# Performance work log

Hardware: AMD Instinct MI355X
Metric: run time of the kernel (lower is better)

The kernel has to match this reference:

```python
import jax, jax.numpy as jnp
import numpy as np

N, F_IN, C, H, E, B = 100000, 128, 64, 4, 1200000, 8
NEG_SLOPE = 0.2
EPS = 1e-5


def setup_inputs() -> dict:
    key = jax.random.key(0)
    ks = jax.random.split(key, 12)
    x = jax.random.normal(ks[0], (N, F_IN), dtype=jnp.float32)
    edge_index = jax.random.randint(ks[1], (2, E), 0, N, dtype=jnp.int64)
    batch = jnp.sort(jax.random.randint(ks[2], (N,), 0, B, dtype=jnp.int64))
    # GATConv params (lin has no bias in PyG)
    W = jax.random.normal(ks[3], (H * C, F_IN), dtype=jnp.float32) / np.sqrt(F_IN)
    att_src = jax.random.normal(ks[4], (H, C), dtype=jnp.float32) / np.sqrt(C)
    att_dst = jax.random.normal(ks[5], (H, C), dtype=jnp.float32) / np.sqrt(C)
    bias_gat = jax.random.normal(ks[6], (C,), dtype=jnp.float32) * 0.02
    # residual projection (in != out)
    res_W = jax.random.normal(ks[7], (C, F_IN), dtype=jnp.float32) / np.sqrt(F_IN)
    res_b = jax.random.normal(ks[8], (C,), dtype=jnp.float32) * 0.02
    # GraphNorm params
    gn_weight = jnp.ones((C,), dtype=jnp.float32) + 0.1 * jax.random.normal(ks[9], (C,), dtype=jnp.float32)
    gn_bias = 0.02 * jax.random.normal(ks[10], (C,), dtype=jnp.float32)
    gn_mean_scale = jnp.ones((C,), dtype=jnp.float32) + 0.1 * jax.random.normal(ks[11], (C,), dtype=jnp.float32)
    return {"x": x, "edge_index": edge_index, "batch": batch, "W": W,
            "att_src": att_src, "att_dst": att_dst, "bias_gat": bias_gat,
            "res_W": res_W, "res_b": res_b, "gn_weight": gn_weight,
            "gn_bias": gn_bias, "gn_mean_scale": gn_mean_scale}


def reference(x, edge_index, batch, W, att_src, att_dst, bias_gat,
              res_W, res_b, gn_weight, gn_bias, gn_mean_scale):
    n = x.shape[0]
    residual = x @ res_W.T + res_b                      # [N, C]
    xl = (x @ W.T).reshape(n, H, C)                     # [N, H, C]
    a_src = jnp.einsum('nhc,hc->nh', xl, att_src)       # [N, H]
    a_dst = jnp.einsum('nhc,hc->nh', xl, att_dst)
    # add self loops
    loop = jnp.arange(n, dtype=edge_index.dtype)
    src = jnp.concatenate([edge_index[0], loop])        # [E+N]
    dst = jnp.concatenate([edge_index[1], loop])
    alpha = jax.nn.leaky_relu(a_src[src] + a_dst[dst], NEG_SLOPE)  # [E+N, H]
    # segment softmax over incoming edges per destination node
    amax = jax.ops.segment_max(alpha, dst, num_segments=n)
    ex = jnp.exp(alpha - amax[dst])
    denom = jax.ops.segment_sum(ex, dst, num_segments=n)
    coef = ex / denom[dst]                              # [E+N, H]
    msg = coef[:, :, None] * xl[src]                    # [E+N, H, C]
    agg = jax.ops.segment_sum(msg, dst, num_segments=n) # [N, H, C]
    out = agg.mean(axis=1) + bias_gat                   # concat=False -> head mean
    h = out + residual
    # GraphNorm over per-graph segments
    cnt = jax.ops.segment_sum(jnp.ones((n,), h.dtype), batch, num_segments=B)[:, None]  # [B,1]
    mean = jax.ops.segment_sum(h, batch, num_segments=B) / cnt                          # [B,C]
    centered = h - mean[batch] * gn_mean_scale
    var = jax.ops.segment_sum(centered * centered, batch, num_segments=B) / cnt         # [B,C]
    normed = gn_weight * centered / jnp.sqrt(var[batch] + EPS) + gn_bias
    return jax.nn.gelu(normed)  # dropout is identity in eval
```

## Files before the change

kernel.cpp:

```cpp
#include <hip/hip_runtime.h>
#include <hip/hip_bf16.h>

typedef __bf16 bf16;
typedef __bf16 bf16x4 __attribute__((ext_vector_type(4)));
typedef __bf16 bf16x8 __attribute__((ext_vector_type(8)));
typedef float floatx4 __attribute__((ext_vector_type(4)));
typedef _Float16 f16;
typedef _Float16 f16x4 __attribute__((ext_vector_type(4)));
typedef _Float16 h2 __attribute__((ext_vector_type(2)));

#define FIN 128
#define HC 256
#define HEADS 4
#define CDIM 64
#define BGRAPH 8
#define NEG 0.2f
#define EPS_GN 1e-5f
#define CAP 48


__device__ __forceinline__ float lrelu(float v) { return v >= 0.f ? v : NEG * v; }
__device__ __forceinline__ float eexp(float v) { return __expf(fminf(v, 60.f)); }

__device__ __forceinline__ float dot2h(h2 a, h2 b, float c) {
#if __has_builtin(__builtin_amdgcn_fdot2)
    return __builtin_amdgcn_fdot2(a, b, c, false);
#else
    return c + (float)a[0] * (float)b[0] + (float)a[1] * (float)b[1];
#endif
}
__device__ __forceinline__ h2 bch2(unsigned u) { return __builtin_bit_cast(h2, u); }

__device__ __forceinline__ bool sniff_i64(const int* __restrict__ p) {
    bool w64 = true;
#pragma unroll
    for (int i = 1; i < 16; i += 2) w64 = w64 && (p[i] == 0);
    return w64;
}
__device__ __forceinline__ bool sniff_f32(const void* __restrict__ xv) {
    const unsigned* u = (const unsigned*)xv;
    bool bf = true;
#pragma unroll
    for (int i = 0; i < 8; ++i) {
        unsigned lo = u[i] & 0xFFFFu;
        unsigned ex = (lo >> 7) & 0xFFu;
        bf = bf && ((ex >= 96u && ex <= 129u) || lo == 0u);
    }
    return !bf;
}

__device__ __forceinline__ int gidx(const int* __restrict__ p, long long i,
                                    bool w64, int hi) {
    long long v = w64 ? ((const long long*)p)[i] : (long long)p[i];
    int x = (int)v;
    return x < 0 ? 0 : (x >= hi ? hi - 1 : x);
}

template <bool F32>
__device__ __forceinline__ float ldf(const void* __restrict__ p, int i) {
    if constexpr (F32) return ((const float*)p)[i];
    else               return (float)((const bf16*)p)[i];
}

template <bool F32>
__device__ __forceinline__ bf16x8 load8(const void* __restrict__ base, size_t off) {
    if constexpr (F32) {
        const float* p = (const float*)base + off;
        float4 a = *(const float4*)p, b = *(const float4*)(p + 4);
        bf16x8 r;
        r[0] = (bf16)a.x; r[1] = (bf16)a.y; r[2] = (bf16)a.z; r[3] = (bf16)a.w;
        r[4] = (bf16)b.x; r[5] = (bf16)b.y; r[6] = (bf16)b.z; r[7] = (bf16)b.w;
        return r;
    } else {
        return *(const bf16x8*)((const bf16*)base + off);
    }
}

template <bool F32>
__device__ __forceinline__ void k1_impl(
        const void* __restrict__ x, const bf16x8* __restrict__ Wlds,
        const void* __restrict__ resW, const void* __restrict__ resB,
        const void* __restrict__ biasG,
        const bf16* __restrict__ aSc, const bf16* __restrict__ aDc,
        f16* __restrict__ xl, float* __restrict__ out_acc,
        float* __restrict__ a_src, float* __restrict__ a_dst, int N) {
    const int wave = threadIdx.x >> 6;
    const int lane = threadIdx.x & 63;
    const int nl = lane & 15;
    const int q  = lane >> 4;
    const int base = blockIdx.x * 128 + wave * 32;

    bf16x8 xf[2][4];
    int nodes[2]; bool g[2];
#pragma unroll
    for (int nt = 0; nt < 2; ++nt) {
        int node = base + nt * 16 + nl;
        nodes[nt] = node; g[nt] = node < N;
        int cn = g[nt] ? node : N - 1;
#pragma unroll
        for (int kq = 0; kq < 4; ++kq)
            xf[nt][kq] = load8<F32>(x, (size_t)cn * FIN + kq * 32 + q * 8);
    }

    float s[2][4] = {{0,0,0,0},{0,0,0,0}};
    float d[2][4] = {{0,0,0,0},{0,0,0,0}};

#pragma unroll
    for (int tile = 0; tile < 16; ++tile) {
        bf16x8 wf[4];
#pragma unroll
        for (int kq = 0; kq < 4; ++kq)
            wf[kq] = Wlds[(tile * 4 + kq) * 64 + lane];
        const int e0 = tile * 16 + q * 4;
        bf16x4 sa = *(const bf16x4*)(aSc + e0);
        bf16x4 da = *(const bf16x4*)(aDc + e0);
#pragma unroll
        for (int nt = 0; nt < 2; ++nt) {
            floatx4 acc = {0,0,0,0};
#pragma unroll
            for (int kq = 0; kq < 4; ++kq)
                acc = __builtin_amdgcn_mfma_f32_16x16x32_bf16(wf[kq], xf[nt][kq], acc, 0, 0, 0);
            f16x4 p;
#pragma unroll
            for (int r = 0; r < 4; ++r) {
                p[r] = (f16)acc[r];
                s[nt][r] += acc[r] * (float)sa[r];
                d[nt][r] += acc[r] * (float)da[r];
            }
            if (g[nt]) *(f16x4*)(xl + (size_t)nodes[nt] * HC + e0) = p;
        }
    }

#pragma unroll
    for (int tile = 0; tile < 4; ++tile) {
        const int R = tile * 16 + nl;
        bf16x8 wf[4];
#pragma unroll
        for (int kq = 0; kq < 4; ++kq)
            wf[kq] = load8<F32>(resW, (size_t)R * FIN + kq * 32 + q * 8);
        const int c0 = tile * 16 + q * 4;
        const float b0 = ldf<F32>(resB, c0 + 0) + ldf<F32>(biasG, c0 + 0);
        const float b1 = ldf<F32>(resB, c0 + 1) + ldf<F32>(biasG, c0 + 1);
        const float b2 = ldf<F32>(resB, c0 + 2) + ldf<F32>(biasG, c0 + 2);
        const float b3 = ldf<F32>(resB, c0 + 3) + ldf<F32>(biasG, c0 + 3);
#pragma unroll
        for (int nt = 0; nt < 2; ++nt) {
            floatx4 acc = {0,0,0,0};
#pragma unroll
            for (int kq = 0; kq < 4; ++kq)
                acc = __builtin_amdgcn_mfma_f32_16x16x32_bf16(wf[kq], xf[nt][kq], acc, 0, 0, 0);
            float4 v = make_float4(acc[0] + b0, acc[1] + b1, acc[2] + b2, acc[3] + b3);
            if (g[nt]) *(float4*)(out_acc + (size_t)nodes[nt] * CDIM + c0) = v;
        }
    }

#pragma unroll
    for (int off = 16; off <= 32; off <<= 1) {
#pragma unroll
        for (int nt = 0; nt < 2; ++nt)
#pragma unroll
            for (int r = 0; r < 4; ++r) {
                s[nt][r] += __shfl_xor(s[nt][r], off, 64);
                d[nt][r] += __shfl_xor(d[nt][r], off, 64);
            }
    }
    if (q == 0) {
#pragma unroll
        for (int nt = 0; nt < 2; ++nt) {
            if (g[nt]) {
                *(float4*)(a_src + (size_t)nodes[nt] * 4) =
                    make_float4(s[nt][0], s[nt][1], s[nt][2], s[nt][3]);
                *(float4*)(a_dst + (size_t)nodes[nt] * 4) =
                    make_float4(d[nt][0], d[nt][1], d[nt][2], d[nt][3]);
            }
        }
    }
}

__global__ __launch_bounds__(256, 2) void k1_gemm(
        const void* __restrict__ x, const void* __restrict__ W,
        const void* __restrict__ resW, const void* __restrict__ resB,
        const void* __restrict__ biasG, const void* __restrict__ attS,
        const void* __restrict__ attD,
        f16* __restrict__ xl, float* __restrict__ out_acc,
        float* __restrict__ a_src, float* __restrict__ a_dst,
        int* __restrict__ cnt, int N) {
    __shared__ bf16x8 Wlds[4096];
    __shared__ bf16 aSc[HC], aDc[HC];
    const bool f32 = sniff_f32(x);
    const int t = threadIdx.x;
    {
        int gid = blockIdx.x * 256 + t;
        if (gid < N) cnt[gid] = 0;
    }
    {
        int src = (t & 3) * 64 + (t >> 2);
        aSc[t] = f32 ? (bf16)((const float*)attS)[src] : ((const bf16*)attS)[src];
        aDc[t] = f32 ? (bf16)((const float*)attD)[src] : ((const bf16*)attD)[src];
    }
    if (f32) {
#pragma unroll
        for (int j = 0; j < 16; ++j) {
            int i = t + j * 256;
            int tileq = i >> 6, lane = i & 63;
            int tile = tileq >> 2, kq = tileq & 3;
            int R = tile * 16 + (lane & 15);
            size_t off = (size_t)((R & 3) * 64 + (R >> 2)) * FIN + kq * 32 + (lane >> 4) * 8;
            Wlds[i] = load8<true>(W, off);
        }
    } else {
#pragma unroll
        for (int j = 0; j < 16; ++j) {
            int i = t + j * 256;
            int tileq = i >> 6, lane = i & 63;
            int tile = tileq >> 2, kq = tileq & 3;
            int R = tile * 16 + (lane & 15);
            size_t off = (size_t)((R & 3) * 64 + (R >> 2)) * FIN + kq * 32 + (lane >> 4) * 8;
            Wlds[i] = load8<false>(W, off);
        }
    }
    __syncthreads();
    if (f32) k1_impl<true >(x, Wlds, resW, resB, biasG, aSc, aDc, xl, out_acc, a_src, a_dst, N);
    else     k1_impl<false>(x, Wlds, resW, resB, biasG, aSc, aDc, xl, out_acc, a_src, a_dst, N);
}

__global__ __launch_bounds__(256) void kscat(
        const int* __restrict__ ei, int* __restrict__ cnt,
        int* __restrict__ adj, int E, int N) {
    int e = blockIdx.x * 256 + threadIdx.x;
    if (e >= E) return;
    bool w64 = sniff_i64(ei);
    int s = gidx(ei, e, w64, N);
    int d = gidx(ei, (long long)E + e, w64, N);
    int pos = atomicAdd(&cnt[d], 1);
    if (pos < CAP) adj[(size_t)d * CAP + pos] = s;
}

__global__ __launch_bounds__(256) void k3_fused(
        const int* __restrict__ cnt, const int* __restrict__ adj,
        const float* __restrict__ a_src, const float* __restrict__ a_dst,
        const f16* __restrict__ xl, float* __restrict__ out_acc, int N) {
    __shared__ unsigned sh_w[4][64][2];
    __shared__ int      sh_off[4][64];
    const int wid  = threadIdx.x >> 6;
    const int lane = threadIdx.x & 63;
    const int n = blockIdx.x * 4 + wid;
    if (n >= N) return;
    int cn = cnt[n]; if (cn > CAP) cn = CAP;
    const float4 ad  = *(const float4*)(a_dst + (size_t)n * 4);
    const float4 asn = *(const float4*)(a_src + (size_t)n * 4);
    const float e0 = eexp(lrelu(asn.x + ad.x));
    const float e1 = eexp(lrelu(asn.y + ad.y));
    const float e2 = eexp(lrelu(asn.z + ad.z));
    const float e3 = eexp(lrelu(asn.w + ad.w));

    float w0 = 0.f, w1 = 0.f, w2 = 0.f, w3 = 0.f;
    float d0 = 0.f, d1 = 0.f, d2 = 0.f, d3 = 0.f;
    int s = 0;
    if (lane < cn) {
        s = adj[(size_t)n * CAP + lane];
        float4 as = *(const float4*)(a_src + (size_t)s * 4);
        w0 = eexp(lrelu(as.x + ad.x));
        w1 = eexp(lrelu(as.y + ad.y));
        w2 = eexp(lrelu(as.z + ad.z));
        w3 = eexp(lrelu(as.w + ad.w));
        d0 = w0; d1 = w1; d2 = w2; d3 = w3;
    }
#pragma unroll
    for (int off = 1; off <= 32; off <<= 1) {
        d0 += __shfl_xor(d0, off, 64);
        d1 += __shfl_xor(d1, off, 64);
        d2 += __shfl_xor(d2, off, 64);
        d3 += __shfl_xor(d3, off, 64);
    }
    d0 += e0; d1 += e1; d2 += e2; d3 += e3;
    const float i0 = 0.25f * __builtin_amdgcn_rcpf(d0);
    const float i1 = 0.25f * __builtin_amdgcn_rcpf(d1);
    const float i2 = 0.25f * __builtin_amdgcn_rcpf(d2);
    const float i3 = 0.25f * __builtin_amdgcn_rcpf(d3);

    if (lane < cn) {
        h2 wa; wa[0] = (f16)(w0 * i0); wa[1] = (f16)(w1 * i1);
        h2 wb; wb[0] = (f16)(w2 * i2); wb[1] = (f16)(w3 * i3);
        sh_w[wid][lane][0] = __builtin_bit_cast(unsigned, wa);
        sh_w[wid][lane][1] = __builtin_bit_cast(unsigned, wb);
        sh_off[wid][lane] = s << 9;
    } else if (lane == cn) {
        h2 wa; wa[0] = (f16)(e0 * i0); wa[1] = (f16)(e1 * i1);
        h2 wb; wb[0] = (f16)(e2 * i2); wb[1] = (f16)(e3 * i3);
        sh_w[wid][cn][0] = __builtin_bit_cast(unsigned, wa);
        sh_w[wid][cn][1] = __builtin_bit_cast(unsigned, wb);
        sh_off[wid][cn] = n << 9;
    }

    const int m = cn + 1;
    const int half = lane >> 5, l32 = lane & 31;
    const char* xb = (const char*)xl + l32 * 16;
    float acc0 = 0.f, acc1 = 0.f;

#define K3DOT(raw, wr) do {                                              \
        h2 va = bch2((raw).x), vb = bch2((raw).y);                       \
        h2 vc = bch2((raw).z), vd = bch2((raw).w);                       \
        h2 wa = bch2((wr).x),  wb = bch2((wr).y);                        \
        acc0 = dot2h(va, wa, acc0); acc0 = dot2h(vb, wb, acc0);          \
        acc1 = dot2h(vc, wa, acc1); acc1 = dot2h(vd, wb, acc1);          \
    } while (0)

    int j = 0;
    for (; j + 4 <= m; j += 4) {
        int offA = sh_off[wid][j + half];
        int offB = sh_off[wid][j + 2 + half];
        uint4 ra = *(const uint4*)(xb + offA);
        uint4 rb = *(const uint4*)(xb + offB);
        uint2 wA = *(const uint2*)&sh_w[wid][j + half][0];
        uint2 wB = *(const uint2*)&sh_w[wid][j + 2 + half][0];
        K3DOT(ra, wA);
        K3DOT(rb, wB);
    }
    if (j + 2 <= m) {
        int offA = sh_off[wid][j + half];
        uint4 ra = *(const uint4*)(xb + offA);
        uint2 wA = *(const uint2*)&sh_w[wid][j + half][0];
        K3DOT(ra, wA);
        j += 2;
    }
    if (j < m && half == 0) {
        int offA = sh_off[wid][j];
        uint4 ra = *(const uint4*)(xb + offA);
        uint2 wA = *(const uint2*)&sh_w[wid][j][0];
        K3DOT(ra, wA);
    }
#undef K3DOT

    acc0 += __shfl_xor(acc0, 32, 64);
    acc1 += __shfl_xor(acc1, 32, 64);
    if (half == 0) {
        float2* p = (float2*)(out_acc + (size_t)n * CDIM + l32 * 2);
        float2 v = *p;
        v.x += acc0; v.y += acc1;
        *p = v;
    }
}

__global__ __launch_bounds__(256) void k4_stats(
        const float* __restrict__ out_acc, const int* __restrict__ batch,
        const int* __restrict__ ei,
        float* __restrict__ pS1, float* __restrict__ pS2, int N) {
    __shared__ float p1[4][BGRAPH][64], p2[4][BGRAPH][64];
    const int w = threadIdx.x >> 6;
    const int c = threadIdx.x & 63;
#pragma unroll
    for (int k = threadIdx.x; k < 4 * BGRAPH * 64; k += 256) {
        ((float*)p1)[k] = 0.f; ((float*)p2)[k] = 0.f;
    }
    __syncthreads();
    bool w64 = sniff_i64(ei);
    const int n0 = blockIdx.x * 256 + w * 64;
    float ls1 = 0.f, ls2 = 0.f;
    int curb = -1;
    for (int i = 0; i < 64; ++i) {
        int n = n0 + i;
        if (n >= N) break;
        float hv = out_acc[(size_t)n * CDIM + c];
        int b = gidx(batch, n, w64, BGRAPH);
        if (b != curb) {
            if (curb >= 0) { p1[w][curb][c] += ls1; p2[w][curb][c] += ls2; }
            curb = b; ls1 = 0.f; ls2 = 0.f;
        }
        ls1 += hv; ls2 += hv * hv;
    }
    if (curb >= 0) { p1[w][curb][c] += ls1; p2[w][curb][c] += ls2; }
    __syncthreads();
    for (int k = threadIdx.x; k < BGRAPH * 64; k += 256) {
        int b = k >> 6, cc = k & 63;
        pS1[(size_t)blockIdx.x * (BGRAPH * 64) + k] =
            p1[0][b][cc] + p1[1][b][cc] + p1[2][b][cc] + p1[3][b][cc];
        pS2[(size_t)blockIdx.x * (BGRAPH * 64) + k] =
            p2[0][b][cc] + p2[1][b][cc] + p2[2][b][cc] + p2[3][b][cc];
    }
}

__global__ __launch_bounds__(256) void kr_reduce(
        const float* __restrict__ pS1, const float* __restrict__ pS2,
        float* __restrict__ S1, float* __restrict__ S2,
        const int* __restrict__ batch, const int* __restrict__ ei,
        int* __restrict__ start, int nblk, int N) {
    __shared__ float r1[4][64], r2[4][64];
    const int b = blockIdx.x;
    const int seg = threadIdx.x >> 6;
    const int c = threadIdx.x & 63;
    float s1 = 0.f, s2 = 0.f;
    for (int blk = seg; blk < nblk; blk += 4) {
        s1 += pS1[(size_t)blk * (BGRAPH * 64) + b * 64 + c];
        s2 += pS2[(size_t)blk * (BGRAPH * 64) + b * 64 + c];
    }
    r1[seg][c] = s1; r2[seg][c] = s2;
    __syncthreads();
    if (seg == 0) {
        S1[b * 64 + c] = r1[0][c] + r1[1][c] + r1[2][c] + r1[3][c];
        S2[b * 64 + c] = r2[0][c] + r2[1][c] + r2[2][c] + r2[3][c];
    }
    if (b == 0 && threadIdx.x <= BGRAPH) {
        int t = threadIdx.x;
        bool w64 = sniff_i64(ei);
        int lo = 0, hi = N;
        while (lo < hi) {
            int mid = (lo + hi) >> 1;
            long long bv = w64 ? ((const long long*)batch)[mid] : (long long)batch[mid];
            if (bv < t) lo = mid + 1; else hi = mid;
        }
        start[t] = lo;
    }
}

template <bool F32>
__device__ __forceinline__ void k6_impl(
        const float* __restrict__ out_acc, const int* __restrict__ batch,
        bool w64,
        const float* __restrict__ S1, const float* __restrict__ S2,
        const int* __restrict__ start, const void* __restrict__ gw,
        const void* __restrict__ gb, const void* __restrict__ msc,
        void* __restrict__ out, int N) {
    int idx = blockIdx.x * 256 + threadIdx.x;
    if (idx >= N * CDIM) return;
    int n = idx >> 6, c = idx & 63;
    int b = gidx(batch, n, w64, BGRAPH);
    int cnt_i = start[b + 1] - start[b];
    float cnt = (float)(cnt_i < 1 ? 1 : cnt_i);
    float m = S1[b * CDIM + c] / cnt;
    float ms = ldf<F32>(msc, c);
    float var = S2[b * CDIM + c] / cnt + m * m * ms * (ms - 2.0f);
    float centered = out_acc[idx] - m * ms;
    float normed = ldf<F32>(gw, c) * centered * rsqrtf(fmaxf(var, 0.f) + EPS_GN)
                   + ldf<F32>(gb, c);
    float t = 0.7978845608028654f * (normed + 0.044715f * normed * normed * normed);
    float gel = 0.5f * normed * (1.0f + tanhf(t));
    if constexpr (F32) ((float*)out)[idx] = gel;
    else               ((bf16*)out)[idx] = (bf16)gel;
}

__global__ __launch_bounds__(256) void k6_norm(
        const void* __restrict__ xsniff,
        const float* __restrict__ out_acc, const int* __restrict__ batch,
        const int* __restrict__ ei,
        const float* __restrict__ S1, const float* __restrict__ S2,
        const int* __restrict__ start, const void* __restrict__ gw,
        const void* __restrict__ gb, const void* __restrict__ msc,
        void* __restrict__ out, int N) {
    bool w64 = sniff_i64(ei);
    if (sniff_f32(xsniff))
        k6_impl<true >(out_acc, batch, w64, S1, S2, start, gw, gb, msc, out, N);
    else
        k6_impl<false>(out_acc, batch, w64, S1, S2, start, gw, gb, msc, out, N);
}

extern "C" void kernel_launch(void* const* d_in, const int* in_sizes, int n_in,
                              void* d_out, int out_size, void* d_ws, size_t ws_size,
                              hipStream_t stream) {
    const void* x     = d_in[0];
    const int*  ei    = (const int*)d_in[1];
    const int*  batch = (const int*)d_in[2];
    const void* W     = d_in[3];
    const void* attS  = d_in[4];
    const void* attD  = d_in[5];
    const void* biasG = d_in[6];
    const void* resW  = d_in[7];
    const void* resB  = d_in[8];
    const void* gw    = d_in[9];
    const void* gb    = d_in[10];
    const void* msc   = d_in[11];

    const int N = in_sizes[0] / FIN;
    const int E = in_sizes[1] / 2;
    const int NB = (N + 255) / 256;

    char* ws = (char*)d_ws;
    size_t off = 0;
    auto alloc = [&](size_t bytes) { char* p = ws + off; off = (off + bytes + 255) & ~(size_t)255; return p; };
    f16*   xl      = (f16*)  alloc((size_t)N * HC * sizeof(f16));
    float* out_acc = (float*)alloc((size_t)N * CDIM * sizeof(float));
    float* a_src   = (float*)alloc((size_t)N * HEADS * sizeof(float));
    float* a_dst   = (float*)alloc((size_t)N * HEADS * sizeof(float));
    int*   cnt     = (int*)  alloc((size_t)N * sizeof(int));
    int*   adj     = (int*)  alloc((size_t)N * CAP * sizeof(int));
    float* pS1     = (float*)alloc((size_t)NB * BGRAPH * 64 * sizeof(float));
    float* pS2     = (float*)alloc((size_t)NB * BGRAPH * 64 * sizeof(float));
    float* S1      = (float*)alloc(BGRAPH * CDIM * sizeof(float));
    float* S2      = (float*)alloc(BGRAPH * CDIM * sizeof(float));
    int*   start   = (int*)  alloc((BGRAPH + 1) * sizeof(int));

    hipLaunchKernelGGL(k1_gemm, dim3((N + 127) / 128), dim3(256), 0, stream,
                       x, W, resW, resB, biasG, attS, attD, xl, out_acc, a_src, a_dst, cnt, N);
    hipLaunchKernelGGL(kscat, dim3((E + 255) / 256), dim3(256), 0, stream, ei, cnt, adj, E, N);
    hipLaunchKernelGGL(k3_fused, dim3((N + 3) / 4), dim3(256), 0, stream,
                       cnt, adj, a_src, a_dst, xl, out_acc, N);
    hipLaunchKernelGGL(k4_stats, dim3(NB), dim3(256), 0, stream,
                       out_acc, batch, ei, pS1, pS2, N);
    hipLaunchKernelGGL(kr_reduce, dim3(BGRAPH), dim3(256), 0, stream,
                       pS1, pS2, S1, S2, batch, ei, start, NB, N);
    hipLaunchKernelGGL(k6_norm, dim3((N * CDIM + 255) / 256), dim3(256), 0, stream,
                       x, out_acc, batch, ei, S1, S2, start, gw, gb, msc, d_out, N);
}
```

Measured before the change: 421.7 us.

## Merge edge scatter into GEMM launch and atomically reduce GraphNorm stats

The edge-scatter kernel becomes extra blocks appended to the GEMM launch, so adjacency building runs alongside the projection GEMM. A small zeroing kernel now clears counters and stat accumulators up front. The per-block partial stats buffer and its separate reduce kernel are replaced by float atomicAdd into the final sums inside k4. This removes a launch and the serial dependency between GEMM and scatter, but the scatter blocks now contend for CU slots with the LDS-heavy GEMM blocks, and the atomic stat reduction is non-deterministic.

```diff
diff --git a/kernel.cpp b/kernel.cpp
--- a/kernel.cpp
+++ b/kernel.cpp
@@ -74,6 +74,14 @@
     } else {
         return *(const bf16x8*)((const bf16*)base + off);
     }
+}
+
+__global__ __launch_bounds__(256) void kz_zero(
+        int* __restrict__ cnt, float* __restrict__ S1,
+        float* __restrict__ S2, int N) {
+    int i = blockIdx.x * 256 + threadIdx.x;
+    if (i < N) cnt[i] = 0;
+    if (i < BGRAPH * CDIM) { S1[i] = 0.f; S2[i] = 0.f; }
 }
 
 template <bool F32>
@@ -184,15 +192,29 @@
         const void* __restrict__ attD,
         f16* __restrict__ xl, float* __restrict__ out_acc,
         float* __restrict__ a_src, float* __restrict__ a_dst,
-        int* __restrict__ cnt, int N) {
+        const int* __restrict__ ei, int* __restrict__ cnt,
+        int* __restrict__ adj, int NB1, int E, int N) {
     __shared__ bf16x8 Wlds[4096];
     __shared__ bf16 aSc[HC], aDc[HC];
+    const int t = threadIdx.x;
+
+    if (blockIdx.x >= NB1) {
+        const long long base = (long long)(blockIdx.x - NB1) * 1024;
+        const bool w64 = sniff_i64(ei);
+#pragma unroll
+        for (int u = 0; u < 4; ++u) {
+            long long e = base + u * 256 + t;
+            if (e < E) {
+                int s = gidx(ei, e, w64, N);
+                int d = gidx(ei, (long long)E + e, w64, N);
+                int pos = atomicAdd(&cnt[d], 1);
+                if (pos < CAP) adj[(size_t)d * CAP + pos] = s;
+            }
+        }
+        return;
+    }
+
     const bool f32 = sniff_f32(x);
-    const int t = threadIdx.x;
-    {
-        int gid = blockIdx.x * 256 + t;
-        if (gid < N) cnt[gid] = 0;
-    }
     {
         int src = (t & 3) * 64 + (t >> 2);
         aSc[t] = f32 ? (bf16)((const float*)attS)[src] : ((const bf16*)attS)[src];
@@ -222,18 +244,6 @@
     __syncthreads();
     if (f32) k1_impl<true >(x, Wlds, resW, resB, biasG, aSc, aDc, xl, out_acc, a_src, a_dst, N);
     else     k1_impl<false>(x, Wlds, resW, resB, biasG, aSc, aDc, xl, out_acc, a_src, a_dst, N);
-}
-
-__global__ __launch_bounds__(256) void kscat(
-        const int* __restrict__ ei, int* __restrict__ cnt,
-        int* __restrict__ adj, int E, int N) {
-    int e = blockIdx.x * 256 + threadIdx.x;
-    if (e >= E) return;
-    bool w64 = sniff_i64(ei);
-    int s = gidx(ei, e, w64, N);
-    int d = gidx(ei, (long long)E + e, w64, N);
-    int pos = atomicAdd(&cnt[d], 1);
-    if (pos < CAP) adj[(size_t)d * CAP + pos] = s;
 }
 
 __global__ __launch_bounds__(256) void k3_fused(
@@ -345,7 +355,8 @@
 __global__ __launch_bounds__(256) void k4_stats(
         const float* __restrict__ out_acc, const int* __restrict__ batch,
         const int* __restrict__ ei,
-        float* __restrict__ pS1, float* __restrict__ pS2, int N) {
+        float* __restrict__ S1, float* __restrict__ S2,
+        int* __restrict__ start, int N) {
     __shared__ float p1[4][BGRAPH][64], p2[4][BGRAPH][64];
     const int w = threadIdx.x >> 6;
     const int c = threadIdx.x & 63;
@@ -373,36 +384,13 @@
     __syncthreads();
     for (int k = threadIdx.x; k < BGRAPH * 64; k += 256) {
         int b = k >> 6, cc = k & 63;
-        pS1[(size_t)blockIdx.x * (BGRAPH * 64) + k] =
-            p1[0][b][cc] + p1[1][b][cc] + p1[2][b][cc] + p1[3][b][cc];
-        pS2[(size_t)blockIdx.x * (BGRAPH * 64) + k] =
-            p2[0][b][cc] + p2[1][b][cc] + p2[2][b][cc] + p2[3][b][cc];
-    }
-}
-
-__global__ __launch_bounds__(256) void kr_reduce(
-        const float* __restrict__ pS1, const float* __restrict__ pS2,
-        float* __restrict__ S1, float* __restrict__ S2,
-        const int* __restrict__ batch, const int* __restrict__ ei,
-        int* __restrict__ start, int nblk, int N) {
-    __shared__ float r1[4][64], r2[4][64];
-    const int b = blockIdx.x;
-    const int seg = threadIdx.x >> 6;
-    const int c = threadIdx.x & 63;
-    float s1 = 0.f, s2 = 0.f;
-    for (int blk = seg; blk < nblk; blk += 4) {
-        s1 += pS1[(size_t)blk * (BGRAPH * 64) + b * 64 + c];
-        s2 += pS2[(size_t)blk * (BGRAPH * 64) + b * 64 + c];
-    }
-    r1[seg][c] = s1; r2[seg][c] = s2;
-    __syncthreads();
-    if (seg == 0) {
-        S1[b * 64 + c] = r1[0][c] + r1[1][c] + r1[2][c] + r1[3][c];
-        S2[b * 64 + c] = r2[0][c] + r2[1][c] + r2[2][c] + r2[3][c];
-    }
-    if (b == 0 && threadIdx.x <= BGRAPH) {
+        float v1 = p1[0][b][cc] + p1[1][b][cc] + p1[2][b][cc] + p1[3][b][cc];
+        float v2 = p2[0][b][cc] + p2[1][b][cc] + p2[2][b][cc] + p2[3][b][cc];
+        if (v1 != 0.f) atomicAdd(&S1[k], v1);
+        if (v2 != 0.f) atomicAdd(&S2[k], v2);
+    }
+    if (blockIdx.x == 0 && threadIdx.x <= BGRAPH) {
         int t = threadIdx.x;
-        bool w64 = sniff_i64(ei);
         int lo = 0, hi = N;
         while (lo < hi) {
             int mid = (lo + hi) >> 1;
@@ -473,6 +461,8 @@
     const int N = in_sizes[0] / FIN;
     const int E = in_sizes[1] / 2;
     const int NB = (N + 255) / 256;
+    const int NB1 = (N + 127) / 128;
+    const int NBS = (E + 1023) / 1024;
 
     char* ws = (char*)d_ws;
     size_t off = 0;
@@ -482,22 +472,20 @@
     float* a_src   = (float*)alloc((size_t)N * HEADS * sizeof(float));
     float* a_dst   = (float*)alloc((size_t)N * HEADS * sizeof(float));
     int*   cnt     = (int*)  alloc((size_t)N * sizeof(int));
-    int*   adj     = (int*)  alloc((size_t)N * CAP * sizeof(int));
-    float* pS1     = (float*)alloc((size_t)NB * BGRAPH * 64 * sizeof(float));
-    float* pS2     = (float*)alloc((size_t)NB * BGRAPH * 64 * sizeof(float));
     float* S1      = (float*)alloc(BGRAPH * CDIM * sizeof(float));
     float* S2      = (float*)alloc(BGRAPH * CDIM * sizeof(float));
+    int*   adj     = (int*)  alloc((size_t)N * CAP * sizeof(int));
     int*   start   = (int*)  alloc((BGRAPH + 1) * sizeof(int));
 
-    hipLaunchKernelGGL(k1_gemm, dim3((N + 127) / 128), dim3(256), 0, stream,
-                       x, W, resW, resB, biasG, attS, attD, xl, out_acc, a_src, a_dst, cnt, N);
-    hipLaunchKernelGGL(kscat, dim3((E + 255) / 256), dim3(256), 0, stream, ei, cnt, adj, E, N);
+    hipLaunchKernelGGL(kz_zero, dim3((N + 255) / 256), dim3(256), 0, stream,
+                       cnt, S1, S2, N);
+    hipLaunchKernelGGL(k1_gemm, dim3(NB1 + NBS), dim3(256), 0, stream,
+                       x, W, resW, resB, biasG, attS, attD, xl, out_acc,
+                       a_src, a_dst, ei, cnt, adj, NB1, E, N);
     hipLaunchKernelGGL(k3_fused, dim3((N + 3) / 4), dim3(256), 0, stream,
                        cnt, adj, a_src, a_dst, xl, out_acc, N);
     hipLaunchKernelGGL(k4_stats, dim3(NB), dim3(256), 0, stream,
-                       out_acc, batch, ei, pS1, pS2, N);
-    hipLaunchKernelGGL(kr_reduce, dim3(BGRAPH), dim3(256), 0, stream,
-                       pS1, pS2, S1, S2, batch, ei, start, NB, N);
+                       out_acc, batch, ei, S1, S2, start, N);
     hipLaunchKernelGGL(k6_norm, dim3((N * CDIM + 255) / 256), dim3(256), 0, stream,
                        x, out_acc, batch, ei, S1, S2, start, gw, gb, msc, d_out, N);
 }
```

New measurement: 372.1 us. 11.8% less time.
